# Kernel tuning notes

Hardware: AMD Instinct MI355X
Metric: run time of the kernel (lower is better)

The kernel has to match this reference:

```python
import jax, jax.numpy as jnp
import numpy as np

SEQ_LEN, BATCH = 200, 4096
VOCAB, EMB_DIM, HID = 50000, 100, 300


def setup_inputs() -> dict:
    key = jax.random.key(0)
    ks = jax.random.split(key, 8)
    s = 0.05  # small init scale to keep tanh unsaturated
    return {
        "x": jax.random.randint(ks[0], (SEQ_LEN, BATCH), 0, VOCAB, dtype=jnp.int64 if jax.config.jax_enable_x64 else jnp.int32),
        "emb": jax.random.normal(ks[1], (VOCAB, EMB_DIM), jnp.float32) * s,
        "W_ih": jax.random.normal(ks[2], (HID, EMB_DIM), jnp.float32) * s,
        "b_ih": jnp.zeros((HID,), jnp.float32),
        "W_hh": jax.random.normal(ks[3], (HID, HID), jnp.float32) * s,
        "b_hh": jnp.zeros((HID,), jnp.float32),
        "W1": jax.random.normal(ks[4], (256, HID), jnp.float32) * s,
        "b1": jnp.zeros((256,), jnp.float32),
        "W2": jax.random.normal(ks[5], (2, 256), jnp.float32) * s,
        "b2": jnp.zeros((2,), jnp.float32),
    }


def reference(x, emb, W_ih, b_ih, W_hh, b_hh, W1, b1, W2, b2):
    # Embedding lookup: [T, B] -> [T, B, E]
    xe = emb[x]
    # Precompute input projections for all timesteps in one big GEMM: [T, B, H]
    xw = jnp.einsum('tbe,he->tbh', xe, W_ih) + b_ih + b_hh
    h0 = jnp.zeros((x.shape[1], W_hh.shape[0]), emb.dtype)

    def step(h, xw_t):
        h = jnp.tanh(xw_t + h @ W_hh.T)  # RNNCell: tanh(x Wih^T + bih + h Whh^T + bhh)
        return h, None

    h, _ = jax.lax.scan(step, h0, xw)
    h = jax.nn.relu(h @ W1.T + b1)
    return h @ W2.T + b2  # [B, 2]
```

## Files before the change

kernel.cpp:

```cpp
#include <hip/hip_runtime.h>

#define SEQ   200
#define BATCH 4096
#define EMB   100
#define HID   300
#define NH1   256
#define BM    16
#define NFRAG 13
#define FRB   14
#define FB    1024
#define BUFB  (FRB * FB)
#define NTMAX 3
#define NHF   10
#define H1P   260
#define PD    5

typedef _Float16 half8 __attribute__((ext_vector_type(8)));
typedef _Float16 half4h __attribute__((ext_vector_type(4)));
typedef float floatx4 __attribute__((ext_vector_type(4)));

__device__ __forceinline__ float fast_tanh(float x) {
    float e = __expf(2.0f * x);
    float r = __builtin_amdgcn_rcpf(e + 1.0f);
    return 1.0f - 2.0f * r;
}

__device__ __forceinline__ int fragoff(int m, int k) {
    return (k >> 5) * FB + ((k >> 3) & 3) * 256 + m * 16 + (k & 7) * 2;
}

__global__ void __launch_bounds__(512)
rnn_fused(const int* __restrict__ x, const float* __restrict__ emb,
          const float* __restrict__ W_ih, const float* __restrict__ b_ih,
          const float* __restrict__ W_hh, const float* __restrict__ b_hh,
          const float* __restrict__ W1, const float* __restrict__ b1,
          const float* __restrict__ W2, const float* __restrict__ b2,
          float* __restrict__ out)
{
    __shared__ __align__(16) _Float16 uf[2][FRB][512];
    __shared__ int      xs[SEQ * BM];
    __shared__ float    h1s[BM][H1P];

    const int tid  = threadIdx.x;
    const int lane = tid & 63;
    const int w    = tid >> 6;
    const int ln15 = lane & 15;
    const int q    = lane >> 4;
    const int row0 = blockIdx.x * BM;

    const int nt = (w < 3) ? 3 : 2;
    const int t0 = (w < 3) ? 3 * w : 2 * w + 3;

    for (int i = tid; i < 2 * FRB * 512 / 2; i += 512) ((unsigned int*)uf)[i] = 0u;
    for (int i = tid; i < SEQ * BM; i += 512)
        xs[i] = x[(size_t)(i >> 4) * BATCH + row0 + (i & 15)];

    half8   Wb[NTMAX][NFRAG];
    floatx4 biasv[NTMAX];
#pragma unroll
    for (int tt = 0; tt < NTMAX; ++tt) {
        const int nb = (t0 + tt) * 16;
#pragma unroll
        for (int r = 0; r < 4; ++r) {
            const int col = nb + 4 * q + r;
            biasv[tt][r] = (col < HID) ? (b_ih[col] + b_hh[col]) : 0.0f;
        }
        const int n = nb + ln15;
#pragma unroll
        for (int kk = 0; kk < NFRAG; ++kk) {
            union { half8 h; unsigned int d[4]; } cv;
#pragma unroll
            for (int j = 0; j < 8; ++j) {
                const int k = kk * 32 + q * 8 + j;
                float v = 0.0f;
                if (n < HID) {
                    if (k < EMB)                        v = W_ih[n * EMB + k];
                    else if (k >= 112 && k < 112 + HID) v = W_hh[n * HID + (k - 112)];
                }
                cv.h[j] = (_Float16)v;
            }
            asm volatile("" : "+v"(cv.d[0]), "+v"(cv.d[1]), "+v"(cv.d[2]), "+v"(cv.d[3]));
            Wb[tt][kk] = cv.h;
        }
    }

    char* ub = (char*)uf;
    const int rdo = lane * 16;
    int hwo[NTMAX];
#pragma unroll
    for (int tt = 0; tt < NTMAX; ++tt)
        hwo[tt] = fragoff(ln15, 112 + (t0 + tt) * 16 + 4 * q);
    const int gr = tid / 25, gc = tid - gr * 25;
    const int xwo = fragoff(gr, 4 * gc);
    __syncthreads();

    if (tid < 400) {
        const int idx = xs[gr];
        const float4 f = ((const float4*)emb)[(size_t)idx * 25 + gc];
        half4h hv; hv[0] = (_Float16)f.x; hv[1] = (_Float16)f.y;
                   hv[2] = (_Float16)f.z; hv[3] = (_Float16)f.w;
        *(half4h*)(ub + xwo) = hv;
    }
    __syncthreads();

    for (int t = 0; t < SEQ; ++t) {
        const int p = t & 1;
        const char* rb = ub + p * BUFB + rdo;
        char*       wb = ub + (1 - p) * BUFB;

        float4 pf;
        const bool do_pf = (t + 1 < SEQ) && (tid < 400);
        if (do_pf) {
            const int idx = xs[(t + 1) * BM + gr];
            pf = ((const float4*)emb)[(size_t)idx * 25 + gc];
        }

        floatx4 acc[NTMAX];
#pragma unroll
        for (int tt = 0; tt < NTMAX; ++tt) acc[tt] = biasv[tt];

        half8 af[NFRAG];
#pragma unroll
        for (int kk = 0; kk < PD; ++kk) af[kk] = *(const half8*)(rb + kk * FB);
#pragma unroll
        for (int kk = 0; kk < NFRAG; ++kk) {
            if (kk + PD < NFRAG) af[kk + PD] = *(const half8*)(rb + (kk + PD) * FB);
#pragma unroll
            for (int tt = 0; tt < NTMAX; ++tt)
                if (tt < nt)
                    acc[tt] = __builtin_amdgcn_mfma_f32_16x16x32_f16(Wb[tt][kk], af[kk], acc[tt], 0, 0, 0);
        }

        if (do_pf) {
            half4h hv; hv[0] = (_Float16)pf.x; hv[1] = (_Float16)pf.y;
                       hv[2] = (_Float16)pf.z; hv[3] = (_Float16)pf.w;
            *(half4h*)(wb + xwo) = hv;
        }
#pragma unroll
        for (int tt = 0; tt < NTMAX; ++tt) {
            if (tt < nt) {
                half4h hv;
#pragma unroll
                for (int r = 0; r < 4; ++r) hv[r] = (_Float16)fast_tanh(acc[tt][r]);
                *(half4h*)(wb + hwo[tt]) = hv;
            }
        }
        __syncthreads();
    }

    {
        const int hro = fragoff(ln15, 112 + q * 8);
        floatx4 hacc[2];
        int ncol[2];
#pragma unroll
        for (int tt = 0; tt < 2; ++tt) {
            const int n = (w * 2 + tt) * 16 + ln15;
            ncol[tt] = n;
            const float b = b1[n];
            hacc[tt][0] = b; hacc[tt][1] = b; hacc[tt][2] = b; hacc[tt][3] = b;
        }
#pragma unroll
        for (int kk = 0; kk < NHF; ++kk) {
            const half8 a = *(const half8*)(ub + hro + kk * FB);
#pragma unroll
            for (int tt = 0; tt < 2; ++tt) {
                half8 bv;
#pragma unroll
                for (int j = 0; j < 8; ++j) {
                    const int k = kk * 32 + q * 8 + j;
                    bv[j] = (_Float16)((k < HID) ? W1[ncol[tt] * HID + k] : 0.0f);
                }
                hacc[tt] = __builtin_amdgcn_mfma_f32_16x16x32_f16(bv, a, hacc[tt], 0, 0, 0);
            }
        }
#pragma unroll
        for (int tt = 0; tt < 2; ++tt) {
            float4 fv;
            fv.x = fmaxf(hacc[tt][0], 0.0f); fv.y = fmaxf(hacc[tt][1], 0.0f);
            fv.z = fmaxf(hacc[tt][2], 0.0f); fv.w = fmaxf(hacc[tt][3], 0.0f);
            *(float4*)&h1s[ln15][(w * 2 + tt) * 16 + 4 * q] = fv;
        }
    }
    __syncthreads();

    if (tid < 32) {
        const int r = tid & 15, o = tid >> 4;
        float a = b2[o];
        const float* ww = W2 + (size_t)o * NH1;
        for (int k = 0; k < NH1; ++k) a += h1s[r][k] * ww[k];
        out[(size_t)(row0 + r) * 2 + o] = a;
    }
}

extern "C" void kernel_launch(void* const* d_in, const int* in_sizes, int n_in,
                              void* d_out, int out_size, void* d_ws, size_t ws_size,
                              hipStream_t stream) {
    const int*   x    = (const int*)d_in[0];
    const float* emb  = (const float*)d_in[1];
    const float* W_ih = (const float*)d_in[2];
    const float* b_ih = (const float*)d_in[3];
    const float* W_hh = (const float*)d_in[4];
    const float* b_hh = (const float*)d_in[5];
    const float* W1   = (const float*)d_in[6];
    const float* b1   = (const float*)d_in[7];
    const float* W2   = (const float*)d_in[8];
    const float* b2   = (const float*)d_in[9];
    float* outp = (float*)d_out;

    hipLaunchKernelGGL(rnn_fused, dim3(BATCH / BM), dim3(512), 0, stream,
                       x, emb, W_ih, b_ih, W_hh, b_hh, W1, b1, W2, b2, outp);
}
```

Baseline: 394.3 us.

## Use 4 waves with 5 column tiles each and prefetch embeddings two steps ahead

```diff
diff --git a/kernel.cpp b/kernel.cpp
--- a/kernel.cpp
+++ b/kernel.cpp
@@ -10,7 +10,7 @@
 #define FRB   14
 #define FB    1024
 #define BUFB  (FRB * FB)
-#define NTMAX 3
+#define NT    5
 #define NHF   10
 #define H1P   260
 #define PD    5
@@ -29,7 +29,7 @@
     return (k >> 5) * FB + ((k >> 3) & 3) * 256 + m * 16 + (k & 7) * 2;
 }
 
-__global__ void __launch_bounds__(512)
+__global__ void __launch_bounds__(256, 1)
 rnn_fused(const int* __restrict__ x, const float* __restrict__ emb,
           const float* __restrict__ W_ih, const float* __restrict__ b_ih,
           const float* __restrict__ W_hh, const float* __restrict__ b_hh,
@@ -47,18 +47,16 @@
     const int ln15 = lane & 15;
     const int q    = lane >> 4;
     const int row0 = blockIdx.x * BM;
-
-    const int nt = (w < 3) ? 3 : 2;
-    const int t0 = (w < 3) ? 3 * w : 2 * w + 3;
-
-    for (int i = tid; i < 2 * FRB * 512 / 2; i += 512) ((unsigned int*)uf)[i] = 0u;
-    for (int i = tid; i < SEQ * BM; i += 512)
+    const int t0   = 5 * w;
+
+    for (int i = tid; i < 2 * FRB * 512 / 2; i += 256) ((unsigned int*)uf)[i] = 0u;
+    for (int i = tid; i < SEQ * BM; i += 256)
         xs[i] = x[(size_t)(i >> 4) * BATCH + row0 + (i & 15)];
 
-    half8   Wb[NTMAX][NFRAG];
-    floatx4 biasv[NTMAX];
-#pragma unroll
-    for (int tt = 0; tt < NTMAX; ++tt) {
+    half8   Wb[NT][NFRAG];
+    floatx4 biasv[NT];
+#pragma unroll
+    for (int tt = 0; tt < NT; ++tt) {
         const int nb = (t0 + tt) * 16;
 #pragma unroll
         for (int r = 0; r < 4; ++r) {
@@ -86,38 +84,49 @@
 
     char* ub = (char*)uf;
     const int rdo = lane * 16;
-    int hwo[NTMAX];
-#pragma unroll
-    for (int tt = 0; tt < NTMAX; ++tt)
+    int hwo[NT];
+#pragma unroll
+    for (int tt = 0; tt < NT; ++tt)
         hwo[tt] = fragoff(ln15, 112 + (t0 + tt) * 16 + 4 * q);
-    const int gr = tid / 25, gc = tid - gr * 25;
-    const int xwo = fragoff(gr, 4 * gc);
+    const int c0 = tid,      c0r = c0 / 25, c0c = c0 - c0r * 25;
+    const int c1 = tid + 256, c1r = c1 / 25, c1c = c1 - c1r * 25;
+    const bool has1 = (c1 < 400);
+    const int xwo0 = fragoff(c0r, c0c * 4);
+    const int xwo1 = has1 ? fragoff(c1r, c1c * 4) : 0;
     __syncthreads();
 
-    if (tid < 400) {
-        const int idx = xs[gr];
-        const float4 f = ((const float4*)emb)[(size_t)idx * 25 + gc];
-        half4h hv; hv[0] = (_Float16)f.x; hv[1] = (_Float16)f.y;
-                   hv[2] = (_Float16)f.z; hv[3] = (_Float16)f.w;
-        *(half4h*)(ub + xwo) = hv;
+    float4 pf0[2][2];
+    {
+        const float4 f0 = ((const float4*)emb)[(size_t)xs[c0r] * 25 + c0c];
+        float4 f1;
+        if (has1) f1 = ((const float4*)emb)[(size_t)xs[c1r] * 25 + c1c];
+        half4h hv; hv[0] = (_Float16)f0.x; hv[1] = (_Float16)f0.y;
+                   hv[2] = (_Float16)f0.z; hv[3] = (_Float16)f0.w;
+        *(half4h*)(ub + xwo0) = hv;
+        if (has1) {
+            half4h h1; h1[0] = (_Float16)f1.x; h1[1] = (_Float16)f1.y;
+                       h1[2] = (_Float16)f1.z; h1[3] = (_Float16)f1.w;
+            *(half4h*)(ub + xwo1) = h1;
+        }
+        pf0[1][0] = ((const float4*)emb)[(size_t)xs[1 * BM + c0r] * 25 + c0c];
+        if (has1) pf0[1][1] = ((const float4*)emb)[(size_t)xs[1 * BM + c1r] * 25 + c1c];
     }
     __syncthreads();
 
+#pragma unroll 2
     for (int t = 0; t < SEQ; ++t) {
         const int p = t & 1;
         const char* rb = ub + p * BUFB + rdo;
         char*       wb = ub + (1 - p) * BUFB;
 
-        float4 pf;
-        const bool do_pf = (t + 1 < SEQ) && (tid < 400);
-        if (do_pf) {
-            const int idx = xs[(t + 1) * BM + gr];
-            pf = ((const float4*)emb)[(size_t)idx * 25 + gc];
-        }
-
-        floatx4 acc[NTMAX];
-#pragma unroll
-        for (int tt = 0; tt < NTMAX; ++tt) acc[tt] = biasv[tt];
+        if (t + 2 < SEQ) {
+            pf0[p][0] = ((const float4*)emb)[(size_t)xs[(t + 2) * BM + c0r] * 25 + c0c];
+            if (has1) pf0[p][1] = ((const float4*)emb)[(size_t)xs[(t + 2) * BM + c1r] * 25 + c1c];
+        }
+
+        floatx4 acc[NT];
+#pragma unroll
+        for (int tt = 0; tt < NT; ++tt) acc[tt] = biasv[tt];
 
         half8 af[NFRAG];
 #pragma unroll
@@ -126,35 +135,39 @@
         for (int kk = 0; kk < NFRAG; ++kk) {
             if (kk + PD < NFRAG) af[kk + PD] = *(const half8*)(rb + (kk + PD) * FB);
 #pragma unroll
-            for (int tt = 0; tt < NTMAX; ++tt)
-                if (tt < nt)
-                    acc[tt] = __builtin_amdgcn_mfma_f32_16x16x32_f16(Wb[tt][kk], af[kk], acc[tt], 0, 0, 0);
-        }
-
-        if (do_pf) {
-            half4h hv; hv[0] = (_Float16)pf.x; hv[1] = (_Float16)pf.y;
-                       hv[2] = (_Float16)pf.z; hv[3] = (_Float16)pf.w;
-            *(half4h*)(wb + xwo) = hv;
-        }
-#pragma unroll
-        for (int tt = 0; tt < NTMAX; ++tt) {
-            if (tt < nt) {
-                half4h hv;
-#pragma unroll
-                for (int r = 0; r < 4; ++r) hv[r] = (_Float16)fast_tanh(acc[tt][r]);
-                *(half4h*)(wb + hwo[tt]) = hv;
+            for (int tt = 0; tt < NT; ++tt)
+                acc[tt] = __builtin_amdgcn_mfma_f32_16x16x32_f16(Wb[tt][kk], af[kk], acc[tt], 0, 0, 0);
+        }
+
+        if (t + 1 < SEQ) {
+            const float4 f0 = pf0[1 - p][0];
+            half4h hv; hv[0] = (_Float16)f0.x; hv[1] = (_Float16)f0.y;
+                       hv[2] = (_Float16)f0.z; hv[3] = (_Float16)f0.w;
+            *(half4h*)(wb + xwo0) = hv;
+            if (has1) {
+                const float4 f1 = pf0[1 - p][1];
+                half4h h1; h1[0] = (_Float16)f1.x; h1[1] = (_Float16)f1.y;
+                           h1[2] = (_Float16)f1.z; h1[3] = (_Float16)f1.w;
+                *(half4h*)(wb + xwo1) = h1;
             }
+        }
+#pragma unroll
+        for (int tt = 0; tt < NT; ++tt) {
+            half4h hv;
+#pragma unroll
+            for (int r = 0; r < 4; ++r) hv[r] = (_Float16)fast_tanh(acc[tt][r]);
+            *(half4h*)(wb + hwo[tt]) = hv;
         }
         __syncthreads();
     }
 
     {
         const int hro = fragoff(ln15, 112 + q * 8);
-        floatx4 hacc[2];
-        int ncol[2];
-#pragma unroll
-        for (int tt = 0; tt < 2; ++tt) {
-            const int n = (w * 2 + tt) * 16 + ln15;
+        floatx4 hacc[4];
+        int ncol[4];
+#pragma unroll
+        for (int tt = 0; tt < 4; ++tt) {
+            const int n = (4 * w + tt) * 16 + ln15;
             ncol[tt] = n;
             const float b = b1[n];
             hacc[tt][0] = b; hacc[tt][1] = b; hacc[tt][2] = b; hacc[tt][3] = b;
@@ -163,7 +176,7 @@
         for (int kk = 0; kk < NHF; ++kk) {
             const half8 a = *(const half8*)(ub + hro + kk * FB);
 #pragma unroll
-            for (int tt = 0; tt < 2; ++tt) {
+            for (int tt = 0; tt < 4; ++tt) {
                 half8 bv;
 #pragma unroll
                 for (int j = 0; j < 8; ++j) {
@@ -174,11 +187,11 @@
             }
         }
 #pragma unroll
-        for (int tt = 0; tt < 2; ++tt) {
+        for (int tt = 0; tt < 4; ++tt) {
             float4 fv;
             fv.x = fmaxf(hacc[tt][0], 0.0f); fv.y = fmaxf(hacc[tt][1], 0.0f);
             fv.z = fmaxf(hacc[tt][2], 0.0f); fv.w = fmaxf(hacc[tt][3], 0.0f);
-            *(float4*)&h1s[ln15][(w * 2 + tt) * 16 + 4 * q] = fv;
+            *(float4*)&h1s[ln15][(4 * w + tt) * 16 + 4 * q] = fv;
         }
     }
     __syncthreads();
@@ -207,6 +220,6 @@
     const float* b2   = (const float*)d_in[9];
     float* outp = (float*)d_out;
 
-    hipLaunchKernelGGL(rnn_fused, dim3(BATCH / BM), dim3(512), 0, stream,
+    hipLaunchKernelGGL(rnn_fused, dim3(BATCH / BM), dim3(256), 0, stream,
                        x, emb, W_ih, b_ih, W_hh, b_hh, W1, b1, W2, b2, outp);
 }
```

New measurement: 479.1 us. 21.5% more time.

## Move embedding prefetch to lighter waves, drop index staging, shorten LDS prefetch

Applied to the files above, without the earlier changes.

```diff
diff --git a/kernel.cpp b/kernel.cpp
--- a/kernel.cpp
+++ b/kernel.cpp
@@ -13,7 +13,7 @@
 #define NTMAX 3
 #define NHF   10
 #define H1P   260
-#define PD    5
+#define PD    3
 
 typedef _Float16 half8 __attribute__((ext_vector_type(8)));
 typedef _Float16 half4h __attribute__((ext_vector_type(4)));
@@ -38,8 +38,7 @@
           float* __restrict__ out)
 {
     __shared__ __align__(16) _Float16 uf[2][FRB][512];
-    __shared__ int      xs[SEQ * BM];
-    __shared__ float    h1s[BM][H1P];
+    __shared__ float h1s[BM][H1P];
 
     const int tid  = threadIdx.x;
     const int lane = tid & 63;
@@ -52,8 +51,6 @@
     const int t0 = (w < 3) ? 3 * w : 2 * w + 3;
 
     for (int i = tid; i < 2 * FRB * 512 / 2; i += 512) ((unsigned int*)uf)[i] = 0u;
-    for (int i = tid; i < SEQ * BM; i += 512)
-        xs[i] = x[(size_t)(i >> 4) * BATCH + row0 + (i & 15)];
 
     half8   Wb[NTMAX][NFRAG];
     floatx4 biasv[NTMAX];
@@ -90,29 +87,48 @@
 #pragma unroll
     for (int tt = 0; tt < NTMAX; ++tt)
         hwo[tt] = fragoff(ln15, 112 + (t0 + tt) * 16 + 4 * q);
-    const int gr = tid / 25, gc = tid - gr * 25;
-    const int xwo = fragoff(gr, 4 * gc);
+
+    const bool st  = (tid >= 192);
+    const int  sc  = tid - 192;
+    const bool st2 = st && (sc < 80);
+    const int  c1  = sc + 320;
+    const int  gr0 = sc / 25, gc0 = sc - gr0 * 25;
+    const int  gr1 = c1 / 25, gc1 = c1 - gr1 * 25;
+    const int  xwo0 = fragoff(gr0 & 15, gc0 * 4);
+    const int  xwo1 = fragoff(gr1 & 15, gc1 * 4);
     __syncthreads();
 
-    if (tid < 400) {
-        const int idx = xs[gr];
-        const float4 f = ((const float4*)emb)[(size_t)idx * 25 + gc];
+    if (st) {
+        const int idx = x[row0 + gr0];
+        const float4 f = ((const float4*)emb)[(size_t)idx * 25 + gc0];
         half4h hv; hv[0] = (_Float16)f.x; hv[1] = (_Float16)f.y;
                    hv[2] = (_Float16)f.z; hv[3] = (_Float16)f.w;
-        *(half4h*)(ub + xwo) = hv;
+        *(half4h*)(ub + xwo0) = hv;
+    }
+    if (st2) {
+        const int idx = x[row0 + gr1];
+        const float4 f = ((const float4*)emb)[(size_t)idx * 25 + gc1];
+        half4h hv; hv[0] = (_Float16)f.x; hv[1] = (_Float16)f.y;
+                   hv[2] = (_Float16)f.z; hv[3] = (_Float16)f.w;
+        *(half4h*)(ub + xwo1) = hv;
     }
     __syncthreads();
 
+#pragma unroll 2
     for (int t = 0; t < SEQ; ++t) {
         const int p = t & 1;
         const char* rb = ub + p * BUFB + rdo;
         char*       wb = ub + (1 - p) * BUFB;
 
-        float4 pf;
-        const bool do_pf = (t + 1 < SEQ) && (tid < 400);
-        if (do_pf) {
-            const int idx = xs[(t + 1) * BM + gr];
-            pf = ((const float4*)emb)[(size_t)idx * 25 + gc];
+        float4 pf0, pf1;
+        const bool has = (t + 1 < SEQ);
+        if (st && has) {
+            const int idx = x[(size_t)(t + 1) * BATCH + row0 + gr0];
+            pf0 = ((const float4*)emb)[(size_t)idx * 25 + gc0];
+        }
+        if (st2 && has) {
+            const int idx = x[(size_t)(t + 1) * BATCH + row0 + gr1];
+            pf1 = ((const float4*)emb)[(size_t)idx * 25 + gc1];
         }
 
         floatx4 acc[NTMAX];
@@ -131,10 +147,15 @@
                     acc[tt] = __builtin_amdgcn_mfma_f32_16x16x32_f16(Wb[tt][kk], af[kk], acc[tt], 0, 0, 0);
         }
 
-        if (do_pf) {
-            half4h hv; hv[0] = (_Float16)pf.x; hv[1] = (_Float16)pf.y;
-                       hv[2] = (_Float16)pf.z; hv[3] = (_Float16)pf.w;
-            *(half4h*)(wb + xwo) = hv;
+        if (st && has) {
+            half4h hv; hv[0] = (_Float16)pf0.x; hv[1] = (_Float16)pf0.y;
+                       hv[2] = (_Float16)pf0.z; hv[3] = (_Float16)pf0.w;
+            *(half4h*)(wb + xwo0) = hv;
+        }
+        if (st2 && has) {
+            half4h hv; hv[0] = (_Float16)pf1.x; hv[1] = (_Float16)pf1.y;
+                       hv[2] = (_Float16)pf1.z; hv[3] = (_Float16)pf1.w;
+            *(half4h*)(wb + xwo1) = hv;
         }
 #pragma unroll
         for (int tt = 0; tt < NTMAX; ++tt) {
```

Measured after the change: 448.1 us. 13.7% more time.
